# Performance work log

Measured on AMD Instinct MI355X. Metric: run time of the kernel, lower is better.

The kernel has to match this reference:

```python
import jax, jax.numpy as jnp
import numpy as np

N, E, D, M, R, NH, HD, FF = 20000, 160000, 64, 4, 5, 4, 16, 16


def _ln(x, g, b, eps=1e-5):
    mu = x.mean(-1, keepdims=True)
    var = ((x - mu) ** 2).mean(-1, keepdims=True)
    return (x - mu) / jnp.sqrt(var + eps) * g + b


def _encoder(x, p):
    # Post-norm nn.TransformerEncoderLayer(D, nhead=4, dim_feedforward=16), eval mode.
    # x: (B, 4, D); returns CLS output (B, D). Padding mask is all-zeros -> no masking.
    B = x.shape[0]
    qkv = x @ p['in_w'].T + p['in_b']                     # (B,4,3D)
    q, k, v = jnp.split(qkv, 3, axis=-1)
    hview = lambda t: t.reshape(B, 4, NH, HD).transpose(0, 2, 1, 3)  # (B,H,4,hd)
    q, k, v = hview(q), hview(k), hview(v)
    attn = jax.nn.softmax(jnp.einsum('bhqd,bhkd->bhqk', q, k) / jnp.sqrt(jnp.float32(HD)), axis=-1)
    o = jnp.einsum('bhqk,bhkd->bhqd', attn, v).transpose(0, 2, 1, 3).reshape(B, 4, D)
    o = o @ p['out_w'].T + p['out_b']
    x = _ln(x + o, p['ln1_g'], p['ln1_b'])
    ff = jax.nn.relu(x @ p['ff1_w'].T + p['ff1_b']) @ p['ff2_w'].T + p['ff2_b']
    x = _ln(x + ff, p['ln2_g'], p['ln2_b'])
    return x[:, 0, :]


def _mem_encode(h_a, h_b, cls_w, sep, p):
    # For each memory slot m: encode [CLS_m, h_a, SEP, h_b]; sum CLS outputs.
    B = h_a.shape[0]
    sep_t = jnp.broadcast_to(sep, (B, 1, D))
    outs = []
    mem_emb = jnp.zeros((B, D), h_a.dtype)
    for m in range(M):  # small fixed loop over memory slots
        cls_t = jnp.broadcast_to(cls_w[m], (B, 1, D))
        seq = jnp.concatenate([cls_t, h_a[:, None, :], sep_t, h_b[:, None, :]], axis=1)
        t = _encoder(seq, p)
        outs.append(t)
        mem_emb = mem_emb + t
    return mem_emb, outs


def setup_inputs() -> dict:
    key = jax.random.key(0)
    ks = jax.random.split(key, 16)
    s = 0.05
    f32 = jnp.float32
    inp = {}
    inp['feat'] = jax.random.normal(ks[0], (N, D), f32)
    inp['src'] = jax.random.randint(ks[1], (E,), 0, N, dtype=jnp.int32)
    inp['dst'] = jax.random.randint(ks[2], (E,), 0, N, dtype=jnp.int32)
    inp['etype'] = jax.random.randint(ks[3], (E,), 0, R, dtype=jnp.int32)
    inp['cls_w'] = jax.random.normal(ks[4], (M, D), f32)           # CLS embedding, std=1 as in source
    inp['sep'] = jax.random.normal(ks[5], (D,), f32)
    inp['in_w'] = jax.random.normal(ks[6], (3 * D, D), f32) * s
    inp['in_b'] = jnp.zeros((3 * D,), f32)
    inp['out_w'] = jax.random.normal(ks[7], (D, D), f32) * s
    inp['out_b'] = jnp.zeros((D,), f32)
    inp['ln1_g'] = jnp.ones((D,), f32)
    inp['ln1_b'] = jnp.zeros((D,), f32)
    inp['ln2_g'] = jnp.ones((D,), f32)
    inp['ln2_b'] = jnp.zeros((D,), f32)
    inp['ff1_w'] = jax.random.normal(ks[8], (FF, D), f32) * s
    inp['ff1_b'] = jnp.zeros((FF,), f32)
    inp['ff2_w'] = jax.random.normal(ks[9], (D, FF), f32) * s
    inp['ff2_b'] = jnp.zeros((D,), f32)
    inp['memcat_w'] = jax.random.normal(ks[10], (M, D), f32) * s
    inp['memcat_b'] = jnp.zeros((M,), f32)
    inp['memw_w'] = jax.random.normal(ks[11], (D * D, D), f32) * s
    inp['h_bias'] = jnp.zeros((D,), f32)
    inp['lnw_g'] = jnp.ones((D,), f32)
    inp['lnw_b'] = jnp.zeros((D,), f32)
    return inp


def reference(feat, src, dst, etype, cls_w, sep, in_w, in_b, out_w, out_b,
              ln1_g, ln1_b, ln2_g, ln2_b, ff1_w, ff1_b, ff2_w, ff2_b,
              memcat_w, memcat_b, memw_w, h_bias, lnw_g, lnw_b):
    p = dict(in_w=in_w, in_b=in_b, out_w=out_w, out_b=out_b, ln1_g=ln1_g, ln1_b=ln1_b,
             ln2_g=ln2_g, ln2_b=ln2_b, ff1_w=ff1_w, ff1_b=ff1_b, ff2_w=ff2_w, ff2_b=ff2_b)
    h_src = feat[src]                                      # (E,D) gather
    h_dst = feat[dst]
    # Per-etype loop in the source uses identical params for every edge, so the message
    # math vectorizes over all edges; only category/label ordering depends on etype.
    mem_emb, outs = _mem_encode(h_src, h_dst, cls_w, sep, p)   # (E,D)
    cat_all = jnp.stack([t @ memcat_w.T + memcat_b for t in outs])  # (M,E,mem_size)
    # Reproduce source ordering: for etype e (ascending), for slot m, edges in original order.
    counts = jnp.bincount(etype, length=R)
    start = jnp.cumsum(counts) - counts                    # exclusive prefix
    perm = jnp.argsort(etype)                              # stable sort by etype
    e_s = etype[perm]
    local = jnp.arange(E) - start[e_s]
    pos = M * start[e_s][None, :] + jnp.arange(M)[:, None] * counts[e_s][None, :] + local[None, :]  # (M,E)
    category = jnp.zeros((M * E, M), cat_all.dtype).at[pos.reshape(-1)].set(cat_all[:, perm].reshape(M * E, M))
    label = jnp.zeros((M * E,), jnp.int32).at[pos.reshape(-1)].set(
        jnp.broadcast_to(jnp.arange(M, dtype=jnp.int32)[:, None], (M, E)).reshape(-1))
    # Dynamic per-edge weight + message
    w = (mem_emb @ memw_w.T).reshape(-1, D, D)             # (E, out, in)
    msg = jnp.einsum('eoi,ei->eo', w, h_src)               # (E,D)
    # fn.mean aggregation (zero-degree nodes -> 0, matching DGL)
    deg = jax.ops.segment_sum(jnp.ones((E,), feat.dtype), dst, num_segments=N)
    agg = jax.ops.segment_sum(msg, dst, num_segments=N) / jnp.maximum(deg, 1.0)[:, None]
    node = _ln(agg, lnw_g, lnw_b) + h_bias
    # self-loop branch: same memory-slot transformer on (feat, feat)
    mem_emb_n, _ = _mem_encode(feat, feat, cls_w, sep, p)
    w_n = (mem_emb_n @ memw_w.T).reshape(-1, D, D)
    node = node + jnp.einsum('noi,ni->no', w_n, feat)
    node = jnp.where(node > 0, node, 0.2 * node)           # LeakyReLU(0.2); dropout is identity in eval
    return node, category, label
```

## Files before the change

### kernel.cpp

```cpp
#include <hip/hip_runtime.h>

#define DI __device__ __forceinline__

static constexpr int NN = 20000;
static constexpr int NE = 160000;

typedef __attribute__((ext_vector_type(4))) float f32x4;
typedef _Float16 f16x2 __attribute__((ext_vector_type(2)));
typedef _Float16 f16x8 __attribute__((ext_vector_type(8)));

DI float rl(float v, int lane) {
    return __int_as_float(__builtin_amdgcn_readlane(__float_as_int(v), lane));
}
DI float xr(float v, int m) { return __shfl_xor(v, m, 64); }
DI int xri(int v, int m) { return __shfl_xor(v, m, 64); }
DI float wsum64(float v) {
    v += xr(v, 1); v += xr(v, 2); v += xr(v, 4);
    v += xr(v, 8); v += xr(v, 16); v += xr(v, 32);
    return v;
}
DI int wsum64i(int v) {
    v += xri(v, 1); v += xri(v, 2); v += xri(v, 4);
    v += xri(v, 8); v += xri(v, 16); v += xri(v, 32);
    return v;
}
DI float hsum16(float v) {
    v += xr(v, 1); v += xr(v, 2); v += xr(v, 4); v += xr(v, 8);
    return v;
}
DI float hsum16d(float v) {
    v += __int_as_float(__builtin_amdgcn_mov_dpp(__float_as_int(v), 0xB1, 0xF, 0xF, true));
    v += __int_as_float(__builtin_amdgcn_mov_dpp(__float_as_int(v), 0x4E, 0xF, 0xF, true));
    v += __int_as_float(__builtin_amdgcn_mov_dpp(__float_as_int(v), 0x141, 0xF, 0xF, true));
    v += __int_as_float(__builtin_amdgcn_mov_dpp(__float_as_int(v), 0x140, 0xF, 0xF, true));
    return v;
}
DI float wsum64v(float v) {
    v = hsum16d(v);
    return (rl(v, 0) + rl(v, 16)) + (rl(v, 32) + rl(v, 48));
}
DI unsigned short f2h(float x) {
    union { _Float16 f; unsigned short u; } c;
    c.f = (_Float16)x;
    return c.u;
}

__global__ __launch_bounds__(256) void prepA_kernel(
    const float* __restrict__ mw, unsigned short* __restrict__ Wstg,
    const float* __restrict__ in_w, const float* __restrict__ out_w,
    float* __restrict__ WOVg,
    const float* __restrict__ cls_w, const float* __restrict__ sep,
    const float* __restrict__ in_b,
    const int* __restrict__ et, int* __restrict__ bc,
    float* __restrict__ agg, float* __restrict__ deg,
    const float* __restrict__ mc_w, const float* __restrict__ mc_b,
    const float* __restrict__ ln1_g, const float* __restrict__ ln1_b,
    const float* __restrict__ ln2_g, const float* __restrict__ ln2_b,
    const float* __restrict__ ff1_w, const float* __restrict__ ff1_b,
    const float* __restrict__ out_b,
    float* __restrict__ SWg, float* __restrict__ SB16,
    float* __restrict__ OvcG, float* __restrict__ OvsG,
    float* __restrict__ bOvG, float* __restrict__ s0n,
    float* __restrict__ s2n, float* __restrict__ MC8,
    float* __restrict__ GcT, float* __restrict__ GsT,
    float* __restrict__ DCC, float* __restrict__ B0T,
    float* __restrict__ mgT) {
    int b = blockIdx.x, t = threadIdx.x;
    __shared__ int c[5];
    __shared__ float P[608];
    if (b < 1024) {
        int idx = b * 256 + t;
        int d = idx & 63, o = (idx >> 6) & 63, i = idx >> 12;
        Wstg[idx] = f2h(mw[(o * 64 + i) * 64 + d]);
    } else if (b < 1088) {
        int u = (b - 1024) * 256 + t;
        int h = u & 3, l = (u >> 2) & 63, j = u >> 8;
        float acc = 0.f;
        for (int i = 0; i < 16; i++)
            acc += out_w[l * 64 + h * 16 + i] * in_w[(128 + h * 16 + i) * 64 + j];
        WOVg[u] = acc;
    } else if (b == 1088) {
        if (t < 64) {
            int l = t;
            float bq = in_b[l], bk = in_b[64 + l], bv = in_b[128 + l];
            float xs = sep[l];
            float ks = bk, vs = bv;
            for (int j = 0; j < 64; j++) {
                float xj = rl(xs, j);
                ks += in_w[(64 + l) * 64 + j] * xj;
                vs += in_w[(128 + l) * 64 + j] * xj;
            }
            P[512 + l] = vs;
            for (int m = 0; m < 4; m++) {
                float xc = cls_w[m * 64 + l];
                float q0 = bq, kc = bk, vc = bv;
                for (int j = 0; j < 64; j++) {
                    float xj = rl(xc, j);
                    q0 += in_w[l * 64 + j] * xj;
                    kc += in_w[(64 + l) * 64 + j] * xj;
                    vc += in_w[(128 + l) * 64 + j] * xj;
                }
                P[m * 64 + l] = q0;
                P[256 + m * 64 + l] = vc;
                float p0 = hsum16(q0 * kc);
                float p2 = hsum16(q0 * ks);
                if ((l & 15) == 0) {
                    P[576 + m * 4 + (l >> 4)] = p0 * 0.25f;
                    P[592 + m * 4 + (l >> 4)] = p2 * 0.25f;
                }
            }
        }
        __syncthreads();
        for (int u = t; u < 1024; u += 256) {
            int m = u >> 8, h = (u >> 6) & 3, j = u & 63;
            float acc = 0.f;
            for (int i = 0; i < 16; i++)
                acc += P[m * 64 + h * 16 + i] * in_w[(64 + h * 16 + i) * 64 + j];
            SWg[u] = 0.25f * acc;
        }
        for (int u = t; u < 1024; u += 256) {
            int h = u & 3, ll = (u >> 2) & 63, m = u >> 8;
            float acc = 0.f;
            for (int i = 0; i < 16; i++)
                acc += out_w[ll * 64 + h * 16 + i] * P[256 + m * 64 + h * 16 + i];
            OvcG[u] = acc;
        }
        if (t < 256) {
            int h = t & 3, ll = t >> 2;
            float a1 = 0.f, a2 = 0.f;
            for (int i = 0; i < 16; i++) {
                a1 += out_w[ll * 64 + h * 16 + i] * P[512 + h * 16 + i];
                a2 += out_w[ll * 64 + h * 16 + i] * in_b[128 + h * 16 + i];
            }
            OvsG[t] = a1;
            bOvG[t] = a2;
        }
        if (t < 256) {
            B0T[t] = cls_w[t] + out_b[t & 63];
            int p = t >> 2, cc = t & 3;
            mgT[t] = mc_w[cc * 64 + p] * ln2_g[p];
        }
        if (t < 16) {
            int m = t >> 2, h = t & 3;
            float acc = 0.f;
            for (int i = 0; i < 16; i++)
                acc += P[m * 64 + h * 16 + i] * in_b[64 + h * 16 + i];
            SB16[t] = 0.25f * acc;
            s0n[t] = P[576 + t];
            s2n[t] = P[592 + t];
        }
        if (t < 8) {
            int cc = t & 3;
            float acc = 0.f;
            if (t < 4) {
                for (int ll = 0; ll < 64; ll++) acc += mc_w[cc * 64 + ll] * ln2_g[ll];
            } else {
                for (int ll = 0; ll < 64; ll++) acc += mc_w[cc * 64 + ll] * ln2_b[ll];
                acc += mc_b[cc];
            }
            MC8[t] = acc;
        }
        __syncthreads();
        if (t < 256) {
            int m = t >> 6, f = (t >> 2) & 15, h = t & 3;
            float acc = 0.f;
            for (int p = 0; p < 64; p++)
                acc += ff1_w[f * 64 + p] * ln1_g[p] * OvcG[(m * 64 + p) * 4 + h];
            GcT[t] = acc;
        }
        if (t < 64) {
            int f = t >> 2, h = t & 3;
            float acc = 0.f;
            for (int p = 0; p < 64; p++)
                acc += ff1_w[f * 64 + p] * ln1_g[p] * OvsG[p * 4 + h];
            GsT[t] = acc;
        }
        if (t < 64) {
            int m = t >> 4, f = t & 15;
            float d0 = 0.f, c1 = 0.f, c2 = 0.f;
            for (int p = 0; p < 64; p++) {
                float wv = ff1_w[f * 64 + p];
                d0 += wv * ln1_g[p] * (cls_w[m * 64 + p] + out_b[p]);
                c1 += wv * ln1_g[p];
                c2 += wv * ln1_b[p];
            }
            f32x4 r = {d0, c1, c2 + ff1_b[f], 0.f};
            ((f32x4*)DCC)[t] = r;
        }
    } else if (b < 1714) {
        int bb = b - 1089;
        if (t < 5) c[t] = 0;
        __syncthreads();
        int e = bb * 256 + t;
        atomicAdd(&c[et[e]], 1);
        __syncthreads();
        if (t < 5) bc[bb * 5 + t] = c[t];
    } else if (b < 2964) {
        int idx = (b - 1714) * 256 + t;
        f32x4 z = {0.f, 0.f, 0.f, 0.f};
        ((f32x4*)agg)[idx] = z;
    } else {
        int idx = (b - 2964) * 256 + t;
        if (idx < 5000) {
            f32x4 z = {0.f, 0.f, 0.f, 0.f};
            ((f32x4*)deg)[idx] = z;
        }
    }
}

__global__ __launch_bounds__(256) void prepC_kernel(
    const int* __restrict__ et, const int* __restrict__ bc,
    const int* __restrict__ dstp, float* __restrict__ deg,
    int* __restrict__ rowbase, int* __restrict__ estride,
    const float* __restrict__ feat, const float* __restrict__ SWg,
    const float* __restrict__ SB16, const float* __restrict__ WOVg,
    const float* __restrict__ bOvG, const float* __restrict__ ff1_w,
    const float* __restrict__ ln1_g,
    float* __restrict__ Sout, float* __restrict__ Ovout, float* __restrict__ Gn) {
    __shared__ float SWs[1024];
    __shared__ f32x4 WOVs[4096];
    __shared__ __align__(16) float F1gL[1024];
    __shared__ __align__(16) float accT[4][4][64];
    __shared__ int wc[4][5];
    __shared__ int pre_s[5], tot_s[5], cs5[5];
    int tid = threadIdx.x;
    if (blockIdx.x < 625) {
        int b = blockIdx.x;
        if (tid < 5) { pre_s[tid] = 0; tot_s[tid] = 0; }
        __syncthreads();
#pragma unroll
        for (int ty = 0; ty < 5; ty++) {
            int pp = 0, tt = 0;
            for (int b2 = tid; b2 < 625; b2 += 256) {
                int v = bc[b2 * 5 + ty];
                tt += v;
                if (b2 < b) pp += v;
            }
            pp = wsum64i(pp);
            tt = wsum64i(tt);
            if ((tid & 63) == 0) {
                atomicAdd(&pre_s[ty], pp);
                atomicAdd(&tot_s[ty], tt);
            }
        }
        __syncthreads();
        if (tid == 0) {
            int s = 0;
            for (int e = 0; e < 5; e++) { cs5[e] = s; s += tot_s[e]; }
        }
        int w = tid >> 6, lane = tid & 63;
        int e = b * 256 + tid;
        int my = et[e];
        unsigned long long bal[5];
#pragma unroll
        for (int ty = 0; ty < 5; ty++) bal[ty] = __ballot(my == ty);
        if (lane == 0) {
#pragma unroll
            for (int ty = 0; ty < 5; ty++) wc[w][ty] = __popcll(bal[ty]);
        }
        __syncthreads();
        unsigned long long lt = ((unsigned long long)1 << lane) - 1;
        int intra = __popcll(bal[my] & lt);
        int pre = 0;
        for (int w2 = 0; w2 < w; w2++) pre += wc[w2][my];
        rowbase[e] = 4 * cs5[my] + pre_s[my] + pre + intra;
        estride[e] = tot_s[my];
        atomicAdd(&deg[dstp[e]], 1.0f);
        return;
    }
    int nb4 = blockIdx.x - 625;
    for (int p = tid; p < 1024; p += 256) {
        SWs[p] = SWg[p];
        F1gL[p] = ff1_w[p] * ln1_g[p & 63];
    }
    for (int p = tid; p < 4096; p += 256) WOVs[p] = ((const f32x4*)WOVg)[p];
    __syncthreads();
    int w = tid >> 6, l = tid & 63;
    int n = nb4 * 4 + w;
    float f = feat[(size_t)n * 64 + l];
    f32x4 acc = ((const f32x4*)bOvG)[l];
#pragma unroll 8
    for (int j = 0; j < 64; j++) {
        float fj = rl(f, j);
        f32x4 wv = WOVs[j * 64 + l];
        acc += wv * fj;
    }
    ((f32x4*)Ovout)[(size_t)n * 64 + l] = acc;
    accT[w][0][l] = acc[0];
    accT[w][1][l] = acc[1];
    accT[w][2][l] = acc[2];
    accT[w][3][l] = acc[3];
#pragma unroll
    for (int mh = 0; mh < 16; mh++) {
        float v = SWs[mh * 64 + l] * f;
        v = wsum64v(v);
        if (l == mh) Sout[(size_t)n * 16 + mh] = v + SB16[mh];
    }
    asm volatile("s_waitcnt lgkmcnt(0)" ::: "memory");
    int ff = l & 15, hh = l >> 4;
    float g = 0.f;
#pragma unroll
    for (int c2 = 0; c2 < 16; c2++) {
        int cc = (c2 + ff) & 15;
        f32x4 wv = *(const f32x4*)&F1gL[ff * 64 + cc * 4];
        f32x4 av = *(const f32x4*)&accT[w][hh][cc * 4];
        g += wv[0] * av[0] + wv[1] * av[1] + wv[2] * av[2] + wv[3] * av[3];
    }
    Gn[(size_t)n * 64 + ff * 4 + hh] = g;
}

__global__ __launch_bounds__(256, 4) void enc_kernel(
    const int* __restrict__ src, const int* __restrict__ dst,
    const float* __restrict__ Sg, const float* __restrict__ Ovg,
    const float* __restrict__ Gn, const float* __restrict__ OvcG,
    const float* __restrict__ OvsG, const float* __restrict__ GcT,
    const float* __restrict__ GsT, const float* __restrict__ DCC,
    const float* __restrict__ B0T, const float* __restrict__ mgT,
    const float* __restrict__ s0n, const float* __restrict__ s2n,
    const float* __restrict__ MC8,
    const float* __restrict__ ln1_g, const float* __restrict__ ln1_b,
    const float* __restrict__ ln2_g, const float* __restrict__ ln2_b,
    const float* __restrict__ ff2_w, const float* __restrict__ ff2_b,
    const int* __restrict__ rowbase, const int* __restrict__ estride,
    float* __restrict__ mem_out, float* __restrict__ out_cat,
    float* __restrict__ out_label) {
    __shared__ __align__(16) float F2C[1024];
    __shared__ __align__(16) float TBL[1704];
    int tid = threadIdx.x;
    for (int p = tid; p < 1024; p += 256) F2C[(p & 15) * 64 + (p >> 4)] = ff2_w[p];
    {
        f32x4* T4w = (f32x4*)TBL;
        int i = tid;
        if (i < 64) {
            T4w[i]        = ((const f32x4*)B0T)[i];
            T4w[64 + i]   = ((const f32x4*)GcT)[i];
            T4w[128 + i]  = ((const f32x4*)DCC)[i];
            T4w[192 + (i & 3) * 16 + (i >> 2)] = ((const f32x4*)OvsG)[i];
            T4w[256 + (i & 3) * 16 + (i >> 2)] = ((const f32x4*)mgT)[i];
        }
        if (i < 16) {
            T4w[320 + i] = ((const f32x4*)GsT)[i];
            T4w[346 + i] = *(const f32x4*)(ln1_g + i * 4);
            T4w[362 + i] = *(const f32x4*)(ln1_b + i * 4);
            T4w[378 + i] = *(const f32x4*)(ln2_g + i * 4);
            T4w[394 + i] = *(const f32x4*)(ln2_b + i * 4);
            T4w[410 + i] = *(const f32x4*)(ff2_b + i * 4);
        }
        if (i < 4) {
            T4w[336 + i] = ((const f32x4*)s0n)[i];
            T4w[340 + i] = ((const f32x4*)s2n)[i];
        }
        if (i < 2) T4w[344 + i] = ((const f32x4*)MC8)[i];
    }
    __syncthreads();
    const f32x4* F2C4 = (const f32x4*)F2C;
    const f32x4* Sg4 = (const f32x4*)Sg;
    const f32x4* Og4 = (const f32x4*)Ovg;
    const f32x4* Gn4 = (const f32x4*)Gn;

    int l = tid & 63, m = l >> 4, u = l & 15;
    f32x4 OvcR0 = ((const f32x4*)OvcG)[m * 64 + u * 4 + 0];
    f32x4 OvcR1 = ((const f32x4*)OvcG)[m * 64 + u * 4 + 1];
    f32x4 OvcR2 = ((const f32x4*)OvcG)[m * 64 + u * 4 + 2];
    f32x4 OvcR3 = ((const f32x4*)OvcG)[m * 64 + u * 4 + 3];
    int ubase = u * 17;
    int wid = blockIdx.x * 4 + (tid >> 6);
    int nw = gridDim.x * 4;

#pragma unroll 2
    for (int it = wid; it < NE + NN; it += nw) {
        int tb = 0;
        asm volatile("" : "+v"(tb));
        const f32x4* T4 = ((const f32x4*)TBL) + tb;
        int itu = __builtin_amdgcn_readfirstlane(it);
        bool isE = itu < NE;
        int ia = isE ? src[itu] : (itu - NE);
        f32x4 SaV = Sg4[(size_t)ia * 4 + m];
        f32x4 GaV = Gn4[(size_t)ia * 16 + u];
        f32x4 OvaR0 = Og4[(size_t)ia * 64 + u * 4 + 0];
        f32x4 OvaR1 = Og4[(size_t)ia * 64 + u * 4 + 1];
        f32x4 OvaR2 = Og4[(size_t)ia * 64 + u * 4 + 2];
        f32x4 OvaR3 = Og4[(size_t)ia * 64 + u * 4 + 3];
        f32x4 SbV = SaV, GbV = GaV;
        f32x4 OvbR0 = OvaR0, OvbR1 = OvaR1, OvbR2 = OvaR2, OvbR3 = OvaR3;
        int rb = 0, st = 0;
        if (isE) {
            int ib = dst[itu];
            SbV = Sg4[(size_t)ib * 4 + m];
            GbV = Gn4[(size_t)ib * 16 + u];
            OvbR0 = Og4[(size_t)ib * 64 + u * 4 + 0];
            OvbR1 = Og4[(size_t)ib * 64 + u * 4 + 1];
            OvbR2 = Og4[(size_t)ib * 64 + u * 4 + 2];
            OvbR3 = Og4[(size_t)ib * 64 + u * 4 + 3];
            rb = rowbase[itu];
            st = estride[itu];
        }
        f32x4 s0v = T4[336 + m];
        f32x4 s2v = T4[340 + m];
        f32x4 B0v = T4[l];
        f32x4 GcV = T4[64 + l];
        f32x4 DCv = T4[128 + l];
        f32x4 GsV = T4[320 + u];
        f32x4 OvsR0 = T4[192 + u];
        f32x4 OvsR1 = T4[208 + u];
        f32x4 OvsR2 = T4[224 + u];
        f32x4 OvsR3 = T4[240 + u];

        f32x4 mx, e0, e1, e2, e3, w0v, w1v, w2v, w3v;
#pragma unroll
        for (int h = 0; h < 4; h++)
            mx[h] = fmaxf(fmaxf(s0v[h], SaV[h]), fmaxf(s2v[h], SbV[h]));
#pragma unroll
        for (int h = 0; h < 4; h++) {
            e0[h] = __expf(s0v[h] - mx[h]);
            e1[h] = __expf(SaV[h] - mx[h]);
            e2[h] = __expf(s2v[h] - mx[h]);
            e3[h] = __expf(SbV[h] - mx[h]);
        }
#pragma unroll
        for (int h = 0; h < 4; h++) {
            float inv = 1.f / (e0[h] + e1[h] + e2[h] + e3[h]);
            w0v[h] = e0[h] * inv; w1v[h] = e1[h] * inv;
            w2v[h] = e2[h] * inv; w3v[h] = e3[h] * inv;
        }
        f32x4 xv = B0v;
#pragma unroll
        for (int h = 0; h < 4; h++) {
            float W0 = w0v[h], W1 = w1v[h], W2 = w2v[h], W3 = w3v[h];
            xv[0] += W0 * OvcR0[h] + W1 * OvaR0[h] + W2 * OvsR0[h] + W3 * OvbR0[h];
            xv[1] += W0 * OvcR1[h] + W1 * OvaR1[h] + W2 * OvsR1[h] + W3 * OvbR1[h];
            xv[2] += W0 * OvcR2[h] + W1 * OvaR2[h] + W2 * OvsR2[h] + W3 * OvbR2[h];
            xv[3] += W0 * OvcR3[h] + W1 * OvaR3[h] + W2 * OvsR3[h] + W3 * OvbR3[h];
        }
        float sx = hsum16d(xv[0] + xv[1] + xv[2] + xv[3]);
        float sxx = hsum16d(xv[0] * xv[0] + xv[1] * xv[1] + xv[2] * xv[2] + xv[3] * xv[3]);
        float mu = sx * 0.015625f;
        float var = sxx * 0.015625f - mu * mu;
        float r1 = rsqrtf(var + 1e-5f);
        f32x4 av = w0v * GcV + w1v * GaV + w2v * GsV + w3v * GbV;
        float accF = av[0] + av[1] + av[2] + av[3] + DCv[0];
        float hp = r1 * accF - (r1 * mu) * DCv[1] + DCv[2];
        float hr = fmaxf(hp, 0.f);
        f32x4 g1r = T4[346 + u], b1r = T4[362 + u], f2br = T4[410 + u];
        xv = (xv - mu) * (g1r * r1) + b1r;
        f32x4 yv = xv + f2br;
        float hrot = hr;
        int a16 = ubase + tb;
        { f32x4 wv = F2C4[a16]; yv += wv * hrot; }
#define FSTEP(CTL, MSK)                                                                         \
        hrot = __int_as_float(__builtin_amdgcn_mov_dpp(__float_as_int(hrot), (CTL), 0xF, 0xF, true)); \
        a16 ^= (MSK) * 16;                                                                      \
        { f32x4 wv = F2C4[a16]; yv += wv * hrot; }
        FSTEP(0xB1, 1) FSTEP(0x4E, 2) FSTEP(0xB1, 1) FSTEP(0x141, 7)
        FSTEP(0xB1, 1) FSTEP(0x4E, 2) FSTEP(0xB1, 1) FSTEP(0x140, 15)
        FSTEP(0xB1, 1) FSTEP(0x4E, 2) FSTEP(0xB1, 1) FSTEP(0x141, 7)
        FSTEP(0xB1, 1) FSTEP(0x4E, 2) FSTEP(0xB1, 1)
#undef FSTEP
        float sy = hsum16d(yv[0] + yv[1] + yv[2] + yv[3]);
        float syy = hsum16d(yv[0] * yv[0] + yv[1] * yv[1] + yv[2] * yv[2] + yv[3] * yv[3]);
        float mu2 = sy * 0.015625f;
        float var2 = syy * 0.015625f - mu2 * mu2;
        float r2 = rsqrtf(var2 + 1e-5f);
        f32x4 g2r = T4[378 + u], b2r = T4[394 + u];
        f32x4 tv = (yv - mu2) * (g2r * r2) + b2r;
        f32x4 mem4;
#pragma unroll
        for (int k = 0; k < 4; k++) {
            float s = tv[k];
            s += xr(s, 16);
            s += xr(s, 32);
            mem4[k] = s;
        }
        if (m == 0) *(f32x4*)(mem_out + (size_t)itu * 64 + u * 4) = mem4;
        if (isE) {
            f32x4 mg0 = T4[256 + u];
            f32x4 mg1 = T4[272 + u];
            f32x4 mg2 = T4[288 + u];
            f32x4 mg3 = T4[304 + u];
            f32x4 pcv = yv[0] * mg0 + yv[1] * mg1 + yv[2] * mg2 + yv[3] * mg3;
            f32x4 McV = T4[344];
            f32x4 CcV = T4[345];
            f32x4 dv;
            dv[0] = hsum16d(pcv[0]);
            dv[1] = hsum16d(pcv[1]);
            dv[2] = hsum16d(pcv[2]);
            dv[3] = hsum16d(pcv[3]);
            f32x4 cv = (dv - McV * mu2) * r2 + CcV;
            int row = rb + m * st;
            if (u == 0) {
                *(f32x4*)(out_cat + (size_t)row * 4) = cv;
                out_label[row] = (float)m;
            }
        }
    }
}

__global__ __launch_bounds__(256, 2) void msg_kernel(
    const float* __restrict__ feat, const int* __restrict__ src, const int* __restrict__ dstv,
    const float* __restrict__ mem_all, const unsigned short* __restrict__ Wstg,
    float* __restrict__ agg, float* __restrict__ msg_n) {
    constexpr int RS = 72;
    constexpr int EB = NE / 256;
    __shared__ __align__(16) unsigned short Wt[4 * 64 * RS];
    __shared__ unsigned hTu[4 * 256];
    int tid = threadIdx.x;
    int w = tid >> 6, lane = tid & 63;
    int m16 = lane & 15, q = lane >> 4;
    bool isE = blockIdx.x < EB;
    int blockbase = (isE ? blockIdx.x : blockIdx.x - EB) * 256;
    int count = isE ? NE : NN;
    size_t moff = isE ? 0 : (size_t)NE;
    int wavebase = w * 64;

    f16x2 mpk[4][2][4];
#pragma unroll
    for (int Mt = 0; Mt < 4; Mt++) {
        int it = blockbase + wavebase + Mt * 16 + m16;
        if (!isE && it >= count) it = count - 1;
        const float* mrow = mem_all + (moff + (size_t)it) * 64;
#pragma unroll
        for (int ks = 0; ks < 2; ks++) {
            float4 a = *(const float4*)(mrow + ks * 32 + q * 8);
            float4 b = *(const float4*)(mrow + ks * 32 + q * 8 + 4);
            mpk[Mt][ks][0] = f16x2{(_Float16)a.x, (_Float16)a.y};
            mpk[Mt][ks][1] = f16x2{(_Float16)a.z, (_Float16)a.w};
            mpk[Mt][ks][2] = f16x2{(_Float16)b.x, (_Float16)b.y};
            mpk[Mt][ks][3] = f16x2{(_Float16)b.z, (_Float16)b.w};
        }
    }
    f32x4 acc[4][4];
#pragma unroll
    for (int Mt = 0; Mt < 4; Mt++)
#pragma unroll
        for (int nt = 0; nt < 4; nt++) {
            f32x4 z = {0.f, 0.f, 0.f, 0.f};
            acc[Mt][nt] = z;
        }

    for (int ch = 0; ch < 16; ch++) {
        __syncthreads();
        const unsigned short* gsl = Wstg + (size_t)ch * 4 * 4096;
#pragma unroll
        for (int p = 0; p < 8; p++) {
            int flat = p * 2048 + tid * 8;
            int ic = flat >> 12, o = (flat >> 6) & 63, d = flat & 63;
            uint4 v = *(const uint4*)(gsl + flat);
            *(uint4*)&Wt[(ic * 64 + o) * RS + d] = v;
        }
        {
            int it = blockbase + tid;
            if (!isE && it >= count) it = count - 1;
            int hidx = isE ? src[it] : it;
            float4 hv = *(const float4*)(feat + (size_t)hidx * 64 + ch * 4);
            union { f16x2 f; unsigned u; } d0, d1, d2, d3;
            d0.f = f16x2{(_Float16)hv.x, (_Float16)hv.x};
            d1.f = f16x2{(_Float16)hv.y, (_Float16)hv.y};
            d2.f = f16x2{(_Float16)hv.z, (_Float16)hv.z};
            d3.f = f16x2{(_Float16)hv.w, (_Float16)hv.w};
            hTu[0 * 256 + tid] = d0.u;
            hTu[1 * 256 + tid] = d1.u;
            hTu[2 * 256 + tid] = d2.u;
            hTu[3 * 256 + tid] = d3.u;
        }
        __syncthreads();

#pragma unroll
        for (int il = 0; il < 4; il++) {
            f16x8 afr[4][2];
#pragma unroll
            for (int Mt = 0; Mt < 4; Mt++) {
                union { f16x2 f; unsigned u; } hh;
                hh.u = hTu[il * 256 + wavebase + Mt * 16 + m16];
                f16x2 hd = hh.f;
#pragma unroll
                for (int ks = 0; ks < 2; ks++) {
                    union { unsigned u[4]; f16x8 v; } uu;
#pragma unroll
                    for (int jj = 0; jj < 4; jj++) {
                        union { f16x2 f; unsigned u; } rr;
                        rr.f = mpk[Mt][ks][jj] * hd;
                        uu.u[jj] = rr.u;
                    }
                    afr[Mt][ks] = uu.v;
                }
            }
            const unsigned short* wrow = &Wt[(il * 64) * RS];
#pragma unroll
            for (int nt = 0; nt < 4; nt++) {
#pragma unroll
                for (int ks = 0; ks < 2; ks++) {
                    int o = nt * 16 + m16;
                    union { uint4 u; f16x8 v; } bb;
                    bb.u = *(const uint4*)&wrow[o * RS + ks * 32 + q * 8];
#pragma unroll
                    for (int Mt = 0; Mt < 4; Mt++)
                        acc[Mt][nt] = __builtin_amdgcn_mfma_f32_16x16x32_f16(
                            afr[Mt][ks], bb.v, acc[Mt][nt], 0, 0, 0);
                }
            }
        }
    }
#pragma unroll
    for (int Mt = 0; Mt < 4; Mt++) {
        int ib = blockbase + wavebase + Mt * 16 + q * 4;
        if (!isE) {
#pragma unroll
            for (int r = 0; r < 4; r++) {
                int it = ib + r;
                if (it < count) {
#pragma unroll
                    for (int nt = 0; nt < 4; nt++)
                        msg_n[(size_t)it * 64 + nt * 16 + m16] = acc[Mt][nt][r];
                }
            }
        } else {
            int4 dd = *(const int4*)(dstv + ib);
#pragma unroll
            for (int r = 0; r < 4; r++) {
                int dn = (&dd.x)[r];
#pragma unroll
                for (int nt = 0; nt < 4; nt++)
                    atomicAdd(&agg[(size_t)dn * 64 + nt * 16 + m16], acc[Mt][nt][r]);
            }
        }
    }
}

__global__ __launch_bounds__(256) void final_kernel(
    const float* __restrict__ agg, const float* __restrict__ deg, const float* __restrict__ msgn,
    const float* __restrict__ lnw_g, const float* __restrict__ lnw_b,
    const float* __restrict__ h_bias, float* __restrict__ outp, int nN) {
    int tid = threadIdx.x, w = tid >> 6, l = tid & 63;
    int n = blockIdx.x * 4 + w;
    if (n >= nN) return;
    float a = agg[(size_t)n * 64 + l] / fmaxf(deg[n], 1.f);
    float mu = wsum64(a) * (1.f / 64.f);
    float d = a - mu;
    float var = wsum64(d * d) * (1.f / 64.f);
    float v = d * rsqrtf(var + 1e-5f) * lnw_g[l] + lnw_b[l] + h_bias[l] + msgn[(size_t)n * 64 + l];
    outp[(size_t)n * 64 + l] = v > 0.f ? v : 0.2f * v;
}


extern "C" void kernel_launch(void* const* d_in, const int* in_sizes, int n_in,
                              void* d_out, int out_size, void* d_ws, size_t ws_size,
                              hipStream_t stream) {
    const float* feat   = (const float*)d_in[0];
    const int*   src    = (const int*)d_in[1];
    const int*   dst    = (const int*)d_in[2];
    const int*   etype  = (const int*)d_in[3];
    const float* cls_w  = (const float*)d_in[4];
    const float* sep    = (const float*)d_in[5];
    const float* in_w   = (const float*)d_in[6];
    const float* in_b   = (const float*)d_in[7];
    const float* out_w  = (const float*)d_in[8];
    const float* out_b  = (const float*)d_in[9];
    const float* ln1_g  = (const float*)d_in[10];
    const float* ln1_b  = (const float*)d_in[11];
    const float* ln2_g  = (const float*)d_in[12];
    const float* ln2_b  = (const float*)d_in[13];
    const float* ff1_w  = (const float*)d_in[14];
    const float* ff1_b  = (const float*)d_in[15];
    const float* ff2_w  = (const float*)d_in[16];
    const float* ff2_b  = (const float*)d_in[17];
    const float* mc_w   = (const float*)d_in[18];
    const float* mc_b   = (const float*)d_in[19];
    const float* memw_w = (const float*)d_in[20];
    const float* h_bias = (const float*)d_in[21];
    const float* lnw_g  = (const float*)d_in[22];
    const float* lnw_b  = (const float*)d_in[23];

    char* ws = (char*)d_ws;
    size_t off = 0;
    auto nxt = [&](size_t bytes) -> void* {
        void* p = ws + off;
        off += (bytes + 255) & ~(size_t)255;
        return p;
    };
    unsigned short* Wstg = (unsigned short*)nxt(64 * 64 * 64 * sizeof(unsigned short));
    float* SWg     = (float*)nxt(1024 * sizeof(float));
    float* SB16    = (float*)nxt(16 * sizeof(float));
    float* OvcG    = (float*)nxt(1024 * sizeof(float));
    float* OvsG    = (float*)nxt(256 * sizeof(float));
    float* bOvG    = (float*)nxt(256 * sizeof(float));
    float* s0n     = (float*)nxt(16 * sizeof(float));
    float* s2n     = (float*)nxt(16 * sizeof(float));
    float* MC8     = (float*)nxt(8 * sizeof(float));
    float* GcT     = (float*)nxt(256 * sizeof(float));
    float* GsT     = (float*)nxt(64 * sizeof(float));
    float* DCC     = (float*)nxt(256 * sizeof(float));
    float* B0T     = (float*)nxt(256 * sizeof(float));
    float* mgT     = (float*)nxt(256 * sizeof(float));
    float* WOVg    = (float*)nxt(16384 * sizeof(float));
    float* Sg      = (float*)nxt((size_t)NN * 16 * sizeof(float));
    float* Ovg     = (float*)nxt((size_t)NN * 256 * sizeof(float));
    float* Gn      = (float*)nxt((size_t)NN * 64 * sizeof(float));
    int*   bc      = (int*)nxt(625 * 5 * sizeof(int));
    int*   rowbase = (int*)nxt((size_t)NE * sizeof(int));
    int*   estride = (int*)nxt((size_t)NE * sizeof(int));
    float* mem_all = (float*)nxt((size_t)(NE + NN) * 64 * sizeof(float));
    float* agg     = (float*)nxt((size_t)NN * 64 * sizeof(float));
    float* deg     = (float*)nxt((size_t)NN * sizeof(float));
    float* msg_n   = (float*)nxt((size_t)NN * 64 * sizeof(float));
    (void)ws_size; (void)in_sizes; (void)n_in; (void)out_size;

    float* out_node  = (float*)d_out;
    float* out_cat   = out_node + (size_t)NN * 64;
    float* out_label = out_cat + (size_t)4 * NE * 4;

    prepA_kernel<<<2984, 256, 0, stream>>>(
        memw_w, Wstg, in_w, out_w, WOVg, cls_w, sep, in_b, etype, bc, agg, deg,
        mc_w, mc_b, ln1_g, ln1_b, ln2_g, ln2_b, ff1_w, ff1_b, out_b,
        SWg, SB16, OvcG, OvsG, bOvG, s0n, s2n, MC8, GcT, GsT, DCC, B0T, mgT);
    prepC_kernel<<<5625, 256, 0, stream>>>(etype, bc, dst, deg, rowbase, estride,
                                           feat, SWg, SB16, WOVg, bOvG, ff1_w, ln1_g,
                                           Sg, Ovg, Gn);
    enc_kernel<<<2048, 256, 0, stream>>>(
        src, dst, Sg, Ovg, Gn, OvcG, OvsG, GcT, GsT, DCC, B0T, mgT, s0n, s2n, MC8,
        ln1_g, ln1_b, ln2_g, ln2_b, ff2_w, ff2_b,
        rowbase, estride, mem_all, out_cat, out_label);
    msg_kernel<<<625 + (NN + 255) / 256, 256, 0, stream>>>(
        feat, src, dst, mem_all, Wstg, agg, msg_n);

    final_kernel<<<(NN + 3) / 4, 256, 0, stream>>>(agg, deg, msg_n, lnw_g, lnw_b, h_bias, out_node, NN);
}
```

Before: 505.6 us.

## Software-pipeline gathered node loads one iteration ahead in memory encode loop

Restructures the per-edge/node loop into a two-stage ping-pong pipeline. The gathers of the next item's scores, O-vectors and G-vectors are issued in the middle of the current item's compute, and the index lookups become unconditional with clamped indices. The goal is to hide the latency of the random global gathers behind arithmetic. In exchange it doubles the live register state, which may lower occupancy or cause spills, and self-loop items now perform redundant loads.

```diff
diff --git a/kernel.cpp b/kernel.cpp
--- a/kernel.cpp
+++ b/kernel.cpp
@@ -366,46 +366,42 @@
     int ubase = u * 17;
     int wid = blockIdx.x * 4 + (tid >> 6);
     int nw = gridDim.x * 4;
-
-#pragma unroll 2
-    for (int it = wid; it < NE + NN; it += nw) {
+    constexpr int TOT = NE + NN;
+
+    struct Side { f32x4 S, G, O0, O1, O2, O3; };
+    struct It2 { Side a, b; int itu, ia, ib, rb, st, isE; };
+    It2 A, B;
+
+    auto PF_S = [&](int pit, It2& n) {
+        int pu = __builtin_amdgcn_readfirstlane(pit);
+        int pe = pu < NE;
+        int sidx = pe ? pu : 0;
+        int ia = pe ? src[sidx] : (pu - NE);
+        int ib = pe ? dst[sidx] : ia;
+        n.itu = pu; n.isE = pe; n.ia = ia; n.ib = ib;
+        n.rb = rowbase[sidx];
+        n.st = estride[sidx];
+        n.a.S = Sg4[(size_t)ia * 4 + m];
+        n.b.S = Sg4[(size_t)ib * 4 + m];
+    };
+    auto PF_O = [&](It2& n) {
+        const f32x4* pa = Og4 + (size_t)n.ia * 64 + u * 4;
+        const f32x4* pb = Og4 + (size_t)n.ib * 64 + u * 4;
+        n.a.O0 = pa[0]; n.a.O1 = pa[1]; n.a.O2 = pa[2]; n.a.O3 = pa[3];
+        n.b.O0 = pb[0]; n.b.O1 = pb[1]; n.b.O2 = pb[2]; n.b.O3 = pb[3];
+    };
+    auto PF_G = [&](It2& n) {
+        n.a.G = Gn4[(size_t)n.ia * 16 + u];
+        n.b.G = Gn4[(size_t)n.ib * 16 + u];
+    };
+
+    auto COMPUTE = [&](It2& c, It2& n, int pit) {
         int tb = 0;
         asm volatile("" : "+v"(tb));
         const f32x4* T4 = ((const f32x4*)TBL) + tb;
-        int itu = __builtin_amdgcn_readfirstlane(it);
-        bool isE = itu < NE;
-        int ia = isE ? src[itu] : (itu - NE);
-        f32x4 SaV = Sg4[(size_t)ia * 4 + m];
-        f32x4 GaV = Gn4[(size_t)ia * 16 + u];
-        f32x4 OvaR0 = Og4[(size_t)ia * 64 + u * 4 + 0];
-        f32x4 OvaR1 = Og4[(size_t)ia * 64 + u * 4 + 1];
-        f32x4 OvaR2 = Og4[(size_t)ia * 64 + u * 4 + 2];
-        f32x4 OvaR3 = Og4[(size_t)ia * 64 + u * 4 + 3];
-        f32x4 SbV = SaV, GbV = GaV;
-        f32x4 OvbR0 = OvaR0, OvbR1 = OvaR1, OvbR2 = OvaR2, OvbR3 = OvaR3;
-        int rb = 0, st = 0;
-        if (isE) {
-            int ib = dst[itu];
-            SbV = Sg4[(size_t)ib * 4 + m];
-            GbV = Gn4[(size_t)ib * 16 + u];
-            OvbR0 = Og4[(size_t)ib * 64 + u * 4 + 0];
-            OvbR1 = Og4[(size_t)ib * 64 + u * 4 + 1];
-            OvbR2 = Og4[(size_t)ib * 64 + u * 4 + 2];
-            OvbR3 = Og4[(size_t)ib * 64 + u * 4 + 3];
-            rb = rowbase[itu];
-            st = estride[itu];
-        }
         f32x4 s0v = T4[336 + m];
         f32x4 s2v = T4[340 + m];
-        f32x4 B0v = T4[l];
-        f32x4 GcV = T4[64 + l];
-        f32x4 DCv = T4[128 + l];
-        f32x4 GsV = T4[320 + u];
-        f32x4 OvsR0 = T4[192 + u];
-        f32x4 OvsR1 = T4[208 + u];
-        f32x4 OvsR2 = T4[224 + u];
-        f32x4 OvsR3 = T4[240 + u];
-
+        f32x4 SaV = c.a.S, SbV = c.b.S;
         f32x4 mx, e0, e1, e2, e3, w0v, w1v, w2v, w3v;
 #pragma unroll
         for (int h = 0; h < 4; h++)
@@ -423,24 +419,35 @@
             w0v[h] = e0[h] * inv; w1v[h] = e1[h] * inv;
             w2v[h] = e2[h] * inv; w3v[h] = e3[h] * inv;
         }
+        PF_S(pit, n);
+        f32x4 B0v = T4[l];
+        f32x4 OvsR0 = T4[192 + u];
+        f32x4 OvsR1 = T4[208 + u];
+        f32x4 OvsR2 = T4[224 + u];
+        f32x4 OvsR3 = T4[240 + u];
         f32x4 xv = B0v;
 #pragma unroll
         for (int h = 0; h < 4; h++) {
             float W0 = w0v[h], W1 = w1v[h], W2 = w2v[h], W3 = w3v[h];
-            xv[0] += W0 * OvcR0[h] + W1 * OvaR0[h] + W2 * OvsR0[h] + W3 * OvbR0[h];
-            xv[1] += W0 * OvcR1[h] + W1 * OvaR1[h] + W2 * OvsR1[h] + W3 * OvbR1[h];
-            xv[2] += W0 * OvcR2[h] + W1 * OvaR2[h] + W2 * OvsR2[h] + W3 * OvbR2[h];
-            xv[3] += W0 * OvcR3[h] + W1 * OvaR3[h] + W2 * OvsR3[h] + W3 * OvbR3[h];
-        }
+            xv[0] += W0 * OvcR0[h] + W1 * c.a.O0[h] + W2 * OvsR0[h] + W3 * c.b.O0[h];
+            xv[1] += W0 * OvcR1[h] + W1 * c.a.O1[h] + W2 * OvsR1[h] + W3 * c.b.O1[h];
+            xv[2] += W0 * OvcR2[h] + W1 * c.a.O2[h] + W2 * OvsR2[h] + W3 * c.b.O2[h];
+            xv[3] += W0 * OvcR3[h] + W1 * c.a.O3[h] + W2 * OvsR3[h] + W3 * c.b.O3[h];
+        }
+        PF_O(n);
         float sx = hsum16d(xv[0] + xv[1] + xv[2] + xv[3]);
         float sxx = hsum16d(xv[0] * xv[0] + xv[1] * xv[1] + xv[2] * xv[2] + xv[3] * xv[3]);
         float mu = sx * 0.015625f;
         float var = sxx * 0.015625f - mu * mu;
         float r1 = rsqrtf(var + 1e-5f);
-        f32x4 av = w0v * GcV + w1v * GaV + w2v * GsV + w3v * GbV;
+        f32x4 GcV = T4[64 + l];
+        f32x4 DCv = T4[128 + l];
+        f32x4 GsV = T4[320 + u];
+        f32x4 av = w0v * GcV + w1v * c.a.G + w2v * GsV + w3v * c.b.G;
         float accF = av[0] + av[1] + av[2] + av[3] + DCv[0];
         float hp = r1 * accF - (r1 * mu) * DCv[1] + DCv[2];
         float hr = fmaxf(hp, 0.f);
+        PF_G(n);
         f32x4 g1r = T4[346 + u], b1r = T4[362 + u], f2br = T4[410 + u];
         xv = (xv - mu) * (g1r * r1) + b1r;
         f32x4 yv = xv + f2br;
@@ -471,8 +478,8 @@
             s += xr(s, 32);
             mem4[k] = s;
         }
-        if (m == 0) *(f32x4*)(mem_out + (size_t)itu * 64 + u * 4) = mem4;
-        if (isE) {
+        if (m == 0) *(f32x4*)(mem_out + (size_t)c.itu * 64 + u * 4) = mem4;
+        if (c.isE) {
             f32x4 mg0 = T4[256 + u];
             f32x4 mg1 = T4[272 + u];
             f32x4 mg2 = T4[288 + u];
@@ -486,12 +493,27 @@
             dv[2] = hsum16d(pcv[2]);
             dv[3] = hsum16d(pcv[3]);
             f32x4 cv = (dv - McV * mu2) * r2 + CcV;
-            int row = rb + m * st;
+            int row = c.rb + m * c.st;
             if (u == 0) {
                 *(f32x4*)(out_cat + (size_t)row * 4) = cv;
                 out_label[row] = (float)m;
             }
         }
+    };
+
+    PF_S(wid, A); PF_O(A); PF_G(A);
+    int it = wid;
+    while (true) {
+        int n1 = it + nw;
+        int p1 = n1 < TOT ? n1 : it;
+        COMPUTE(A, B, p1);
+        if (n1 >= TOT) break;
+        it = n1;
+        int n2 = it + nw;
+        int p2 = n2 < TOT ? n2 : it;
+        COMPUTE(B, A, p2);
+        if (n2 >= TOT) break;
+        it = n2;
     }
 }
 
```

Measured after the change: 553.1 us. +9.4%, slower.

## Replace atomic scatter aggregation with CSR-style per-destination gather

Applied to the files above, without the earlier changes.

Replaces the float atomicAdd scatter of per-edge messages into agg with a counting-sort build of per-destination edge lists (count, prefix scan, fill). msg_kernel now writes messages in place into mem_all, and final_kernel gathers and averages them per node. This removes the 64-wide float atomics per edge and the zeroing of agg/deg. In exchange it adds integer atomics, a single-block serial scan, and irregular gathers in final_kernel. The fill order from atomics is nondeterministic, so summation order can vary between runs.

```diff
diff --git a/kernel.cpp b/kernel.cpp
--- a/kernel.cpp
+++ b/kernel.cpp
@@ -52,7 +52,7 @@
     const float* __restrict__ cls_w, const float* __restrict__ sep,
     const float* __restrict__ in_b,
     const int* __restrict__ et, int* __restrict__ bc,
-    float* __restrict__ agg, float* __restrict__ deg,
+    const int* __restrict__ dstp, int* __restrict__ cnt,
     const float* __restrict__ mc_w, const float* __restrict__ mc_b,
     const float* __restrict__ ln1_g, const float* __restrict__ ln1_b,
     const float* __restrict__ ln2_g, const float* __restrict__ ln2_b,
@@ -195,23 +195,16 @@
         atomicAdd(&c[et[e]], 1);
         __syncthreads();
         if (t < 5) bc[bb * 5 + t] = c[t];
-    } else if (b < 2964) {
-        int idx = (b - 1714) * 256 + t;
-        f32x4 z = {0.f, 0.f, 0.f, 0.f};
-        ((f32x4*)agg)[idx] = z;
     } else {
-        int idx = (b - 2964) * 256 + t;
-        if (idx < 5000) {
-            f32x4 z = {0.f, 0.f, 0.f, 0.f};
-            ((f32x4*)deg)[idx] = z;
-        }
+        int e = (b - 1714) * 256 + t;
+        atomicAdd(&cnt[dstp[e]], 1);
     }
 }
 
 __global__ __launch_bounds__(256) void prepC_kernel(
     const int* __restrict__ et, const int* __restrict__ bc,
-    const int* __restrict__ dstp, float* __restrict__ deg,
     int* __restrict__ rowbase, int* __restrict__ estride,
+    const int* __restrict__ cnt, int* __restrict__ basep,
     const float* __restrict__ feat, const float* __restrict__ SWg,
     const float* __restrict__ SB16, const float* __restrict__ WOVg,
     const float* __restrict__ bOvG, const float* __restrict__ ff1_w,
@@ -223,7 +216,30 @@
     __shared__ __align__(16) float accT[4][4][64];
     __shared__ int wc[4][5];
     __shared__ int pre_s[5], tot_s[5], cs5[5];
+    __shared__ int part[256];
     int tid = threadIdx.x;
+    if (blockIdx.x == 5625) {
+        constexpr int CH = 79;
+        int s0 = tid * CH;
+        int sum = 0;
+        for (int i = 0; i < CH; i++) {
+            int idx = s0 + i;
+            if (idx < NN) sum += cnt[idx];
+        }
+        part[tid] = sum;
+        __syncthreads();
+        if (tid == 0) {
+            int run = 0;
+            for (int i = 0; i < 256; i++) { int v = part[i]; part[i] = run; run += v; }
+        }
+        __syncthreads();
+        int run = part[tid];
+        for (int i = 0; i < CH; i++) {
+            int idx = s0 + i;
+            if (idx < NN) { basep[idx] = run; run += cnt[idx]; }
+        }
+        return;
+    }
     if (blockIdx.x < 625) {
         int b = blockIdx.x;
         if (tid < 5) { pre_s[tid] = 0; tot_s[tid] = 0; }
@@ -265,7 +281,6 @@
         for (int w2 = 0; w2 < w; w2++) pre += wc[w2][my];
         rowbase[e] = 4 * cs5[my] + pre_s[my] + pre + intra;
         estride[e] = tot_s[my];
-        atomicAdd(&deg[dstp[e]], 1.0f);
         return;
     }
     int nb4 = blockIdx.x - 625;
@@ -322,11 +337,19 @@
     const float* __restrict__ ln2_g, const float* __restrict__ ln2_b,
     const float* __restrict__ ff2_w, const float* __restrict__ ff2_b,
     const int* __restrict__ rowbase, const int* __restrict__ estride,
+    const int* __restrict__ basep, int* __restrict__ curs, int* __restrict__ elist,
     float* __restrict__ mem_out, float* __restrict__ out_cat,
     float* __restrict__ out_label) {
+    int tid = threadIdx.x;
+    if (blockIdx.x >= 2048) {
+        int e = (blockIdx.x - 2048) * 256 + tid;
+        int d = dst[e];
+        int pos = basep[d] + atomicAdd(&curs[d], 1);
+        elist[pos] = e;
+        return;
+    }
     __shared__ __align__(16) float F2C[1024];
     __shared__ __align__(16) float TBL[1704];
-    int tid = threadIdx.x;
     for (int p = tid; p < 1024; p += 256) F2C[(p & 15) * 64 + (p >> 4)] = ff2_w[p];
     {
         f32x4* T4w = (f32x4*)TBL;
@@ -365,7 +388,7 @@
     f32x4 OvcR3 = ((const f32x4*)OvcG)[m * 64 + u * 4 + 3];
     int ubase = u * 17;
     int wid = blockIdx.x * 4 + (tid >> 6);
-    int nw = gridDim.x * 4;
+    constexpr int nw = 2048 * 4;
 
 #pragma unroll 2
     for (int it = wid; it < NE + NN; it += nw) {
@@ -496,9 +519,8 @@
 }
 
 __global__ __launch_bounds__(256, 2) void msg_kernel(
-    const float* __restrict__ feat, const int* __restrict__ src, const int* __restrict__ dstv,
-    const float* __restrict__ mem_all, const unsigned short* __restrict__ Wstg,
-    float* __restrict__ agg, float* __restrict__ msg_n) {
+    const float* __restrict__ feat, const int* __restrict__ src,
+    float* __restrict__ mem_all, const unsigned short* __restrict__ Wstg) {
     constexpr int RS = 72;
     constexpr int EB = NE / 256;
     __shared__ __align__(16) unsigned short Wt[4 * 64 * RS];
@@ -603,41 +625,38 @@
 #pragma unroll
     for (int Mt = 0; Mt < 4; Mt++) {
         int ib = blockbase + wavebase + Mt * 16 + q * 4;
-        if (!isE) {
-#pragma unroll
-            for (int r = 0; r < 4; r++) {
-                int it = ib + r;
-                if (it < count) {
-#pragma unroll
-                    for (int nt = 0; nt < 4; nt++)
-                        msg_n[(size_t)it * 64 + nt * 16 + m16] = acc[Mt][nt][r];
-                }
-            }
-        } else {
-            int4 dd = *(const int4*)(dstv + ib);
-#pragma unroll
-            for (int r = 0; r < 4; r++) {
-                int dn = (&dd.x)[r];
+#pragma unroll
+        for (int r = 0; r < 4; r++) {
+            int it = ib + r;
+            if (it < count) {
 #pragma unroll
                 for (int nt = 0; nt < 4; nt++)
-                    atomicAdd(&agg[(size_t)dn * 64 + nt * 16 + m16], acc[Mt][nt][r]);
+                    mem_all[(moff + (size_t)it) * 64 + nt * 16 + m16] = acc[Mt][nt][r];
             }
         }
     }
 }
 
 __global__ __launch_bounds__(256) void final_kernel(
-    const float* __restrict__ agg, const float* __restrict__ deg, const float* __restrict__ msgn,
+    const int* __restrict__ cnt, const int* __restrict__ basep,
+    const int* __restrict__ elist, const float* __restrict__ mem_all,
     const float* __restrict__ lnw_g, const float* __restrict__ lnw_b,
     const float* __restrict__ h_bias, float* __restrict__ outp, int nN) {
     int tid = threadIdx.x, w = tid >> 6, l = tid & 63;
     int n = blockIdx.x * 4 + w;
     if (n >= nN) return;
-    float a = agg[(size_t)n * 64 + l] / fmaxf(deg[n], 1.f);
+    int cn = cnt[n], bs = basep[n];
+    float a = 0.f;
+    for (int j = 0; j < cn; j++) {
+        int e = elist[bs + j];
+        a += mem_all[(size_t)e * 64 + l];
+    }
+    a /= fmaxf((float)cn, 1.f);
     float mu = wsum64(a) * (1.f / 64.f);
     float d = a - mu;
     float var = wsum64(d * d) * (1.f / 64.f);
-    float v = d * rsqrtf(var + 1e-5f) * lnw_g[l] + lnw_b[l] + h_bias[l] + msgn[(size_t)n * 64 + l];
+    float msgn = mem_all[((size_t)NE + n) * 64 + l];
+    float v = d * rsqrtf(var + 1e-5f) * lnw_g[l] + lnw_b[l] + h_bias[l] + msgn;
     outp[(size_t)n * 64 + l] = v > 0.f ? v : 0.2f * v;
 }
 
@@ -698,29 +717,31 @@
     int*   bc      = (int*)nxt(625 * 5 * sizeof(int));
     int*   rowbase = (int*)nxt((size_t)NE * sizeof(int));
     int*   estride = (int*)nxt((size_t)NE * sizeof(int));
+    int*   cnt     = (int*)nxt((size_t)2 * NN * sizeof(int));
+    int*   curs    = cnt + NN;
+    int*   basep   = (int*)nxt((size_t)NN * sizeof(int));
+    int*   elist   = (int*)nxt((size_t)NE * sizeof(int));
     float* mem_all = (float*)nxt((size_t)(NE + NN) * 64 * sizeof(float));
-    float* agg     = (float*)nxt((size_t)NN * 64 * sizeof(float));
-    float* deg     = (float*)nxt((size_t)NN * sizeof(float));
-    float* msg_n   = (float*)nxt((size_t)NN * 64 * sizeof(float));
     (void)ws_size; (void)in_sizes; (void)n_in; (void)out_size;
 
     float* out_node  = (float*)d_out;
     float* out_cat   = out_node + (size_t)NN * 64;
     float* out_label = out_cat + (size_t)4 * NE * 4;
 
-    prepA_kernel<<<2984, 256, 0, stream>>>(
-        memw_w, Wstg, in_w, out_w, WOVg, cls_w, sep, in_b, etype, bc, agg, deg,
+    hipMemsetAsync(cnt, 0, (size_t)2 * NN * sizeof(int), stream);
+
+    prepA_kernel<<<2339, 256, 0, stream>>>(
+        memw_w, Wstg, in_w, out_w, WOVg, cls_w, sep, in_b, etype, bc, dst, cnt,
         mc_w, mc_b, ln1_g, ln1_b, ln2_g, ln2_b, ff1_w, ff1_b, out_b,
         SWg, SB16, OvcG, OvsG, bOvG, s0n, s2n, MC8, GcT, GsT, DCC, B0T, mgT);
-    prepC_kernel<<<5625, 256, 0, stream>>>(etype, bc, dst, deg, rowbase, estride,
+    prepC_kernel<<<5626, 256, 0, stream>>>(etype, bc, rowbase, estride, cnt, basep,
                                            feat, SWg, SB16, WOVg, bOvG, ff1_w, ln1_g,
                                            Sg, Ovg, Gn);
-    enc_kernel<<<2048, 256, 0, stream>>>(
+    enc_kernel<<<2673, 256, 0, stream>>>(
         src, dst, Sg, Ovg, Gn, OvcG, OvsG, GcT, GsT, DCC, B0T, mgT, s0n, s2n, MC8,
         ln1_g, ln1_b, ln2_g, ln2_b, ff2_w, ff2_b,
-        rowbase, estride, mem_all, out_cat, out_label);
-    msg_kernel<<<625 + (NN + 255) / 256, 256, 0, stream>>>(
-        feat, src, dst, mem_all, Wstg, agg, msg_n);
-
-    final_kernel<<<(NN + 3) / 4, 256, 0, stream>>>(agg, deg, msg_n, lnw_g, lnw_b, h_bias, out_node, NN);
-}
+        rowbase, estride, basep, curs, elist, mem_all, out_cat, out_label);
+    msg_kernel<<<625 + (NN + 255) / 256, 256, 0, stream>>>(feat, src, mem_all, Wstg);
+    final_kernel<<<(NN + 3) / 4, 256, 0, stream>>>(cnt, basep, elist, mem_all,
+                                                   lnw_g, lnw_b, h_bias, out_node, NN);
+}
```

After: 540.0 us. +6.8%, slower.

## Drop LDS staging in msg_kernel; read weights from global and shuffle h

Applied to the files above, without the earlier changes.

Removes the shared-memory staging of the weight tiles and of the per-edge source features in msg_kernel, along with both __syncthreads per chunk. Weight fragments are now loaded directly from global memory, relying on L1/L2 since every block reads the same weights. Per-row h values are distributed across lanes with wave shuffles. Launch bounds rise to 3 blocks per SM for more occupancy, at the cost of more global/L2 traffic per MFMA and possible register pressure.

```diff
diff --git a/kernel.cpp b/kernel.cpp
--- a/kernel.cpp
+++ b/kernel.cpp
@@ -495,14 +495,11 @@
     }
 }
 
-__global__ __launch_bounds__(256, 2) void msg_kernel(
+__global__ __launch_bounds__(256, 3) void msg_kernel(
     const float* __restrict__ feat, const int* __restrict__ src, const int* __restrict__ dstv,
     const float* __restrict__ mem_all, const unsigned short* __restrict__ Wstg,
     float* __restrict__ agg, float* __restrict__ msg_n) {
-    constexpr int RS = 72;
     constexpr int EB = NE / 256;
-    __shared__ __align__(16) unsigned short Wt[4 * 64 * RS];
-    __shared__ unsigned hTu[4 * 256];
     int tid = threadIdx.x;
     int w = tid >> 6, lane = tid & 63;
     int m16 = lane & 15, q = lane >> 4;
@@ -537,40 +534,29 @@
             acc[Mt][nt] = z;
         }
 
+    int hit = blockbase + tid;
+    if (!isE && hit >= count) hit = count - 1;
+    int hidx = isE ? src[hit] : hit;
+    const float* hrow = feat + (size_t)hidx * 64;
+
     for (int ch = 0; ch < 16; ch++) {
-        __syncthreads();
-        const unsigned short* gsl = Wstg + (size_t)ch * 4 * 4096;
-#pragma unroll
-        for (int p = 0; p < 8; p++) {
-            int flat = p * 2048 + tid * 8;
-            int ic = flat >> 12, o = (flat >> 6) & 63, d = flat & 63;
-            uint4 v = *(const uint4*)(gsl + flat);
-            *(uint4*)&Wt[(ic * 64 + o) * RS + d] = v;
-        }
+        float4 hv = *(const float4*)(hrow + ch * 4);
+        unsigned hpk[4];
         {
-            int it = blockbase + tid;
-            if (!isE && it >= count) it = count - 1;
-            int hidx = isE ? src[it] : it;
-            float4 hv = *(const float4*)(feat + (size_t)hidx * 64 + ch * 4);
-            union { f16x2 f; unsigned u; } d0, d1, d2, d3;
-            d0.f = f16x2{(_Float16)hv.x, (_Float16)hv.x};
-            d1.f = f16x2{(_Float16)hv.y, (_Float16)hv.y};
-            d2.f = f16x2{(_Float16)hv.z, (_Float16)hv.z};
-            d3.f = f16x2{(_Float16)hv.w, (_Float16)hv.w};
-            hTu[0 * 256 + tid] = d0.u;
-            hTu[1 * 256 + tid] = d1.u;
-            hTu[2 * 256 + tid] = d2.u;
-            hTu[3 * 256 + tid] = d3.u;
-        }
-        __syncthreads();
-
+            union { f16x2 f; unsigned u; } cc;
+            cc.f = f16x2{(_Float16)hv.x, (_Float16)hv.x}; hpk[0] = cc.u;
+            cc.f = f16x2{(_Float16)hv.y, (_Float16)hv.y}; hpk[1] = cc.u;
+            cc.f = f16x2{(_Float16)hv.z, (_Float16)hv.z}; hpk[2] = cc.u;
+            cc.f = f16x2{(_Float16)hv.w, (_Float16)hv.w}; hpk[3] = cc.u;
+        }
 #pragma unroll
         for (int il = 0; il < 4; il++) {
+            const unsigned short* wtile = Wstg + (size_t)(ch * 4 + il) * 4096;
             f16x8 afr[4][2];
 #pragma unroll
             for (int Mt = 0; Mt < 4; Mt++) {
                 union { f16x2 f; unsigned u; } hh;
-                hh.u = hTu[il * 256 + wavebase + Mt * 16 + m16];
+                hh.u = (unsigned)__shfl((int)hpk[il], Mt * 16 + m16, 64);
                 f16x2 hd = hh.f;
 #pragma unroll
                 for (int ks = 0; ks < 2; ks++) {
@@ -584,14 +570,13 @@
                     afr[Mt][ks] = uu.v;
                 }
             }
-            const unsigned short* wrow = &Wt[(il * 64) * RS];
 #pragma unroll
             for (int nt = 0; nt < 4; nt++) {
+                int o = nt * 16 + m16;
 #pragma unroll
                 for (int ks = 0; ks < 2; ks++) {
-                    int o = nt * 16 + m16;
                     union { uint4 u; f16x8 v; } bb;
-                    bb.u = *(const uint4*)&wrow[o * RS + ks * 32 + q * 8];
+                    bb.u = *(const uint4*)&wtile[o * 64 + ks * 32 + q * 8];
 #pragma unroll
                     for (int Mt = 0; Mt < 4; Mt++)
                         acc[Mt][nt] = __builtin_amdgcn_mfma_f32_16x16x32_f16(
```

After: 631.2 us. +24.8%, slower.
